# Kernel optimization log

Hardware: AMD Instinct MI355X
Metric: run time of the kernel (lower is better)

## Reference

```python
import jax, jax.numpy as jnp
import numpy as np

NEG_BIG = -1e9

def setup_inputs() -> dict:
    key = jax.random.key(0)
    kq, kk, kv, kwq, kwk, kwv, km = jax.random.split(key, 7)
    B, S, d = 16, 1024, 512
    Q = jax.random.normal(kq, (B, S, d), dtype=jnp.float32)
    K = jax.random.normal(kk, (B, S, d), dtype=jnp.float32)
    V = jax.random.normal(kv, (B, S, d), dtype=jnp.float32)
    # nn.Linear weights [d, d]; torch applies x @ W.T
    WQ = jax.random.normal(kwq, (d, d), dtype=jnp.float32) / np.sqrt(d)
    WK = jax.random.normal(kwk, (d, d), dtype=jnp.float32) / np.sqrt(d)
    WV = jax.random.normal(kwv, (d, d), dtype=jnp.float32) / np.sqrt(d)
    mask = jax.random.randint(km, (B, S), 0, 2, dtype=jnp.int32)
    return {"Q": Q, "K": K, "V": V, "WQ": WQ, "WK": WK, "WV": WV, "mask": mask}


def reference(Q, K, V, WQ, WK, WV, mask):
    d = Q.shape[-1]
    q = jnp.einsum('bsd,ed->bse', Q, WQ)
    k = jnp.einsum('bsd,ed->bse', K, WK)
    v = jnp.einsum('bsd,ed->bse', V, WV)
    scores = jnp.einsum('bqd,bkd->bqk', q, k) / jnp.sqrt(jnp.float32(d))
    attn = jax.nn.softmax(scores, axis=-1)
    # Faithful to original: mask applied AFTER softmax with -1e9 fill
    m = mask[:, None, :]  # [B,1,S] broadcast over query dim
    attn = jnp.where(m == 0, jnp.float32(NEG_BIG), attn)
    out = jnp.einsum('bqk,bkd->bqd', attn, v)
    return (out, attn)
```

## Files before the change

kernel.cpp:

```cpp
#include <hip/hip_runtime.h>
#include <hip/hip_bf16.h>

typedef float f32x4 __attribute__((ext_vector_type(4)));
typedef __bf16 bf16x8 __attribute__((ext_vector_type(8)));
typedef unsigned short u16x8 __attribute__((ext_vector_type(8)));
typedef unsigned short u16x4 __attribute__((ext_vector_type(4)));
typedef int i32x4 __attribute__((ext_vector_type(4)));

#define NEG_BIG_F (-1000000000.0f)
#define SCALE_F 0.044194173824159216f

__device__ __forceinline__ unsigned short f2bf(float f) {
  unsigned int u = __float_as_uint(f);
  u += 0x7FFFu + ((u >> 16) & 1u);
  return (unsigned short)(u >> 16);
}

__device__ __forceinline__ float bf2f(unsigned short h) {
  return __uint_as_float((unsigned int)h << 16);
}

__device__ __forceinline__ u16x8 cvt8(f32x4 a, f32x4 b) {
  u16x8 r;
  r[0] = f2bf(a[0]); r[1] = f2bf(a[1]); r[2] = f2bf(a[2]); r[3] = f2bf(a[3]);
  r[4] = f2bf(b[0]); r[5] = f2bf(b[1]); r[6] = f2bf(b[2]); r[7] = f2bf(b[3]);
  return r;
}

__device__ __forceinline__ void gload16(const void* g, char* l) {
  __builtin_amdgcn_global_load_lds(
      (const __attribute__((address_space(1))) unsigned int*)g,
      (__attribute__((address_space(3))) unsigned int*)l, 16, 0, 0);
}

__global__ __launch_bounds__(256) void cvtW(
    const float* __restrict__ w0, const float* __restrict__ w1,
    const float* __restrict__ w2, unsigned short* __restrict__ out)
{
  const float* src = blockIdx.z == 0 ? w0 : (blockIdx.z == 1 ? w1 : w2);
  unsigned short* dst = out + (size_t)blockIdx.z * 262144;
  const int i = (blockIdx.x * 256 + threadIdx.x) * 8;
  f32x4 a = *(const f32x4*)(src + i);
  f32x4 b = *(const f32x4*)(src + i + 4);
  *(u16x8*)&dst[i] = cvt8(a, b);
}

__global__ __launch_bounds__(512, 2) void proj_all(
    const float* __restrict__ Q, const float* __restrict__ Kx,
    const float* __restrict__ V, const unsigned short* __restrict__ wb,
    unsigned short* __restrict__ qb, unsigned short* __restrict__ kb,
    unsigned short* __restrict__ vt)
{
  __shared__ __align__(16) unsigned short lds[32768];

  const int bid = blockIdx.x;
  const int tid = threadIdx.x;
  const int lane = tid & 63, wave = tid >> 6;
  const int fr = lane & 15, fq = lane >> 4;

  if (bid < 256) {
    const int z = bid >> 7, rem = bid & 127;
    const float* X = z ? Kx : Q;
    const unsigned short* W = wb + (size_t)z * 262144;
    unsigned short* Y = z ? kb : qb;
    const int m0 = (rem & 63) * 256, n0 = (rem >> 6) * 256;
    const int wr = (wave >> 2) * 128, wc = (wave & 3) * 64;

    unsigned short (*As)[256][32] = (unsigned short (*)[256][32])lds;
    unsigned short (*Bs)[256][32] = (unsigned short (*)[256][32])(lds + 16384);

    f32x4 acc[8][4] = {};

    int arow_s[2], aswz_s[2];
    const float* gAs[2];
    #pragma unroll
    for (int i = 0; i < 2; i++) {
      const int c = tid + 512 * i;
      arow_s[i] = c >> 2;
      aswz_s[i] = ((c & 3) ^ ((arow_s[i] >> 1) & 3)) * 8;
      gAs[i] = X + (size_t)(m0 + arow_s[i]) * 512 + (c & 3) * 8;
    }
    const unsigned short* gB[2]; char* lB[2];
    #pragma unroll
    for (int i = 0; i < 2; i++) {
      const int c = tid + 512 * i, row = c >> 2, slot = c & 3;
      gB[i] = W + (size_t)(n0 + row) * 512 + (slot ^ ((row >> 1) & 3)) * 8;
      lB[i] = (char*)(lds + 16384) + c * 16;
    }

    f32x4 pa[2][2][2];
    #pragma unroll
    for (int i = 0; i < 2; i++) {
      pa[0][i][0] = *(const f32x4*)(gAs[i]);
      pa[0][i][1] = *(const f32x4*)(gAs[i] + 4);
      pa[1][i][0] = *(const f32x4*)(gAs[i] + 32);
      pa[1][i][1] = *(const f32x4*)(gAs[i] + 36);
    }
    #pragma unroll
    for (int i = 0; i < 2; i++) gload16(gB[i], lB[i]);
    #pragma unroll
    for (int i = 0; i < 2; i++)
      *(u16x8*)&As[0][arow_s[i]][aswz_s[i]] = cvt8(pa[0][i][0], pa[0][i][1]);

    #pragma unroll
    for (int t = 0; t < 16; t++) {
      const int cur = t & 1, nxt = cur ^ 1;
      const int kt = t * 32;
      if (t < 15) {
        #pragma unroll
        for (int i = 0; i < 2; i++) gload16(gB[i] + kt + 32, lB[i] + nxt * 16384);
      }
      if (t < 14) {
        #pragma unroll
        for (int i = 0; i < 2; i++) {
          pa[cur][i][0] = *(const f32x4*)(gAs[i] + kt + 64);
          pa[cur][i][1] = *(const f32x4*)(gAs[i] + kt + 68);
        }
      }
      if (t == 0 || t == 14)
        asm volatile("s_waitcnt vmcnt(6) lgkmcnt(0)" ::: "memory");
      else if (t == 15)
        asm volatile("s_waitcnt vmcnt(0) lgkmcnt(0)" ::: "memory");
      else
        asm volatile("s_waitcnt vmcnt(10) lgkmcnt(0)" ::: "memory");
      __builtin_amdgcn_sched_barrier(0);
      __builtin_amdgcn_s_barrier();

      bf16x8 bv[4];
      #pragma unroll
      for (int nf = 0; nf < 4; nf++) {
        const int br = wc + nf * 16 + fr;
        bv[nf] = *(const bf16x8*)&Bs[cur][br][(fq ^ ((br >> 1) & 3)) * 8];
      }
      #pragma unroll
      for (int mf = 0; mf < 8; mf++) {
        const int ar = wr + mf * 16 + fr;
        bf16x8 av = *(const bf16x8*)&As[cur][ar][(fq ^ ((ar >> 1) & 3)) * 8];
        #pragma unroll
        for (int nf = 0; nf < 4; nf++)
          acc[mf][nf] = __builtin_amdgcn_mfma_f32_16x16x32_bf16(av, bv[nf], acc[mf][nf], 0, 0, 0);
      }

      if (t < 15) {
        #pragma unroll
        for (int i = 0; i < 2; i++)
          *(u16x8*)&As[nxt][arow_s[i]][aswz_s[i]] = cvt8(pa[nxt][i][0], pa[nxt][i][1]);
      }
      __builtin_amdgcn_s_barrier();
    }

    #pragma unroll
    for (int mf = 0; mf < 8; mf++)
      #pragma unroll
      for (int nf = 0; nf < 4; nf++)
        #pragma unroll
        for (int rr = 0; rr < 4; rr++) {
          const int m = m0 + wr + mf * 16 + fq * 4 + rr;
          const int n = n0 + wc + nf * 16 + fr;
          Y[(size_t)m * 512 + n] = f2bf(acc[mf][nf][rr]);
        }
  } else {
    const int c0 = bid - 256;
    const int m0 = (c0 & 3) * 128, n0 = ((c0 >> 2) & 3) * 256, b = c0 >> 4;
    const int wr = (wave >> 2) * 64, wc = (wave & 3) * 64;
    const unsigned short* wv = wb + 524288;

    unsigned short (*As)[128][32] = (unsigned short (*)[128][32])lds;
    unsigned short (*Bs)[256][32] = (unsigned short (*)[256][32])(lds + 8192);

    f32x4 acc[4][4] = {};

    const int ar_s = tid >> 2, aslot = tid & 3;
    const unsigned short* gA = wv + (size_t)(m0 + ar_s) * 512 + (aslot ^ ((ar_s >> 1) & 3)) * 8;
    char* lA = (char*)lds + tid * 16;

    int brow_s[2], bswz_s[2];
    const float* gBs[2];
    #pragma unroll
    for (int i = 0; i < 2; i++) {
      const int c = tid + 512 * i;
      brow_s[i] = c >> 2;
      bswz_s[i] = ((c & 3) ^ ((brow_s[i] >> 1) & 3)) * 8;
      gBs[i] = V + ((size_t)b * 1024 + n0 + brow_s[i]) * 512 + (c & 3) * 8;
    }

    f32x4 pb[2][2][2];
    #pragma unroll
    for (int i = 0; i < 2; i++) {
      pb[0][i][0] = *(const f32x4*)(gBs[i]);
      pb[0][i][1] = *(const f32x4*)(gBs[i] + 4);
      pb[1][i][0] = *(const f32x4*)(gBs[i] + 32);
      pb[1][i][1] = *(const f32x4*)(gBs[i] + 36);
    }
    gload16(gA, lA);
    #pragma unroll
    for (int i = 0; i < 2; i++)
      *(u16x8*)&Bs[0][brow_s[i]][bswz_s[i]] = cvt8(pb[0][i][0], pb[0][i][1]);

    #pragma unroll
    for (int t = 0; t < 16; t++) {
      const int cur = t & 1, nxt = cur ^ 1;
      const int kt = t * 32;
      if (t < 15) gload16(gA + kt + 32, lA + nxt * 8192);
      if (t < 14) {
        #pragma unroll
        for (int i = 0; i < 2; i++) {
          pb[cur][i][0] = *(const f32x4*)(gBs[i] + kt + 64);
          pb[cur][i][1] = *(const f32x4*)(gBs[i] + kt + 68);
        }
      }
      if (t == 0 || t == 14)
        asm volatile("s_waitcnt vmcnt(5) lgkmcnt(0)" ::: "memory");
      else if (t == 15)
        asm volatile("s_waitcnt vmcnt(0) lgkmcnt(0)" ::: "memory");
      else
        asm volatile("s_waitcnt vmcnt(9) lgkmcnt(0)" ::: "memory");
      __builtin_amdgcn_sched_barrier(0);
      __builtin_amdgcn_s_barrier();

      bf16x8 av[4], bv[4];
      #pragma unroll
      for (int mf = 0; mf < 4; mf++) {
        const int ar = wr + mf * 16 + fr;
        av[mf] = *(const bf16x8*)&As[cur][ar][(fq ^ ((ar >> 1) & 3)) * 8];
      }
      #pragma unroll
      for (int nf = 0; nf < 4; nf++) {
        const int br = wc + nf * 16 + fr;
        bv[nf] = *(const bf16x8*)&Bs[cur][br][(fq ^ ((br >> 1) & 3)) * 8];
      }
      #pragma unroll
      for (int mf = 0; mf < 4; mf++)
        #pragma unroll
        for (int nf = 0; nf < 4; nf++)
          acc[mf][nf] = __builtin_amdgcn_mfma_f32_16x16x32_bf16(av[mf], bv[nf], acc[mf][nf], 0, 0, 0);

      if (t < 15) {
        #pragma unroll
        for (int i = 0; i < 2; i++)
          *(u16x8*)&Bs[nxt][brow_s[i]][bswz_s[i]] = cvt8(pb[nxt][i][0], pb[nxt][i][1]);
      }
      __builtin_amdgcn_s_barrier();
    }

    #pragma unroll
    for (int mf = 0; mf < 4; mf++)
      #pragma unroll
      for (int nf = 0; nf < 4; nf++)
        #pragma unroll
        for (int rr = 0; rr < 4; rr++) {
          const int e = m0 + wr + mf * 16 + fq * 4 + rr;
          const int s = n0 + wc + nf * 16 + fr;
          vt[((size_t)b * 512 + e) * 1024 + s] = f2bf(acc[mf][nf][rr]);
        }
  }
}

__global__ __launch_bounds__(512, 2) void score_mv(
    const unsigned short* __restrict__ qb, const unsigned short* __restrict__ kb,
    const unsigned short* __restrict__ vt, const int* __restrict__ mask,
    unsigned short* __restrict__ P, float* __restrict__ partial,
    float* __restrict__ mvsum)
{
  __shared__ __align__(16) unsigned short As[2][256][32];
  __shared__ __align__(16) unsigned short Bs[2][256][32];

  const int bid = blockIdx.x;
  const int tid = threadIdx.x;

  if (bid >= 256) {
    const int row = (bid - 256) * 8 + (tid >> 6);
    const int b = row >> 9;
    const int lane = tid & 63;
    const unsigned short* vr = vt + (size_t)row * 1024 + lane * 16;
    const int* mr = mask + b * 1024 + lane * 16;
    u16x8 v0 = *(const u16x8*)(vr);
    u16x8 v1 = *(const u16x8*)(vr + 8);
    float s = 0.f;
    #pragma unroll
    for (int j = 0; j < 8; j++) {
      if (!mr[j])     s += bf2f(v0[j]);
      if (!mr[8 + j]) s += bf2f(v1[j]);
    }
    #pragma unroll
    for (int o = 32; o > 0; o >>= 1) s += __shfl_xor(s, o);
    if (lane == 0) mvsum[row] = s;
    return;
  }

  const int bz = bid >> 4;
  const int m0 = (bid & 3) * 256, n0 = ((bid >> 2) & 3) * 256;
  const int lane = tid & 63, wave = tid >> 6;
  const int wr = (wave >> 2) * 128, wc = (wave & 3) * 64;
  const int fr = lane & 15, fq = lane >> 4;

  f32x4 acc[8][4] = {};

  const unsigned short* gA[2]; char* lA[2];
  const unsigned short* gB[2]; char* lB[2];
  #pragma unroll
  for (int i = 0; i < 2; i++) {
    const int c = tid + 512 * i, row = c >> 2, slot = c & 3;
    const int sw = (slot ^ ((row >> 1) & 3)) * 8;
    gA[i] = qb + ((size_t)bz * 1024 + m0 + row) * 512 + sw;
    gB[i] = kb + ((size_t)bz * 1024 + n0 + row) * 512 + sw;
    lA[i] = (char*)&As[0][0][0] + c * 16;
    lB[i] = (char*)&Bs[0][0][0] + c * 16;
  }

  #pragma unroll
  for (int i = 0; i < 2; i++) { gload16(gA[i], lA[i]); gload16(gB[i], lB[i]); }

  int cur = 0;
  for (int kt = 0; kt < 512; kt += 32) {
    const int nb = cur ^ 1;
    if (kt < 480) {
      #pragma unroll
      for (int i = 0; i < 2; i++) {
        gload16(gA[i] + kt + 32, lA[i] + nb * 16384);
        gload16(gB[i] + kt + 32, lB[i] + nb * 16384);
      }
      asm volatile("s_waitcnt vmcnt(4) lgkmcnt(0)" ::: "memory");
    } else {
      asm volatile("s_waitcnt vmcnt(0) lgkmcnt(0)" ::: "memory");
    }
    __builtin_amdgcn_sched_barrier(0);
    __builtin_amdgcn_s_barrier();

    bf16x8 bv[4];
    #pragma unroll
    for (int nf = 0; nf < 4; nf++) {
      const int br = wc + nf * 16 + fr;
      bv[nf] = *(const bf16x8*)&Bs[cur][br][(fq ^ ((br >> 1) & 3)) * 8];
    }
    #pragma unroll
    for (int mf = 0; mf < 8; mf++) {
      const int ar = wr + mf * 16 + fr;
      bf16x8 av = *(const bf16x8*)&As[cur][ar][(fq ^ ((ar >> 1) & 3)) * 8];
      #pragma unroll
      for (int nf = 0; nf < 4; nf++)
        acc[mf][nf] = __builtin_amdgcn_mfma_f32_16x16x32_bf16(av, bv[nf], acc[mf][nf], 0, 0, 0);
    }
    __builtin_amdgcn_s_barrier();
    cur = nb;
  }

  int mcol[4];
  #pragma unroll
  for (int nf = 0; nf < 4; nf++)
    mcol[nf] = mask[bz * 1024 + n0 + wc + nf * 16 + fr];

  unsigned short* Pb = P + ((size_t)bz << 20);
  const int slot = ((bid >> 2) & 3) * 4 + (wave & 3);
  #pragma unroll
  for (int mf = 0; mf < 8; mf++) {
    #pragma unroll
    for (int rr = 0; rr < 4; rr++) {
      const int m = m0 + wr + mf * 16 + fq * 4 + rr;
      float e = 0.f;
      #pragma unroll
      for (int nf = 0; nf < 4; nf++) {
        const float ev = __expf(acc[mf][nf][rr] * SCALE_F);
        e += ev;
        Pb[(size_t)m * 1024 + n0 + wc + nf * 16 + fr] =
            mcol[nf] ? f2bf(ev) : (unsigned short)0;
      }
      e += __shfl_xor(e, 1); e += __shfl_xor(e, 2);
      e += __shfl_xor(e, 4); e += __shfl_xor(e, 8);
      if (fr == 0)
        partial[(size_t)slot * 16384 + bz * 1024 + m] = e;
    }
  }
}

__global__ __launch_bounds__(512) void pv_attn(
    const unsigned short* __restrict__ P, const unsigned short* __restrict__ vt,
    const float* __restrict__ partial, const float* __restrict__ mvsum,
    const int* __restrict__ mask,
    float* __restrict__ out, float* __restrict__ attn)
{
  __shared__ __align__(16) unsigned short As[2][64][32];
  __shared__ __align__(16) unsigned short Bs[2][512][32];
  __shared__ float inv_l[64];

  const int tid = threadIdx.x;
  const int bz = blockIdx.z, m0 = blockIdx.x * 64;
  const int lane = tid & 63, wave = tid >> 6;
  const int n0 = wave * 64;
  const int fr = lane & 15, fq = lane >> 4;

  f32x4 acc[4][4] = {};

  if (tid < 64) {
    float s = 0.f;
    #pragma unroll
    for (int p = 0; p < 16; p++) s += partial[(size_t)p * 16384 + bz * 1024 + m0 + tid];
    inv_l[tid] = 1.0f / s;
  }

  const unsigned short* gA = nullptr; char* lA = nullptr;
  if (tid < 256) {
    const int row = tid >> 2, slot = tid & 3;
    gA = P + ((size_t)bz << 20) + (size_t)(m0 + row) * 1024 + (slot ^ ((row >> 1) & 3)) * 8;
    lA = (char*)&As[0][0][0] + tid * 16;
  }
  const unsigned short* gB[4]; char* lB[4];
  #pragma unroll
  for (int i = 0; i < 4; i++) {
    const int c = tid + 512 * i, row = c >> 2, slot = c & 3;
    gB[i] = vt + ((size_t)bz * 512 + row) * 1024 + (slot ^ ((row >> 1) & 3)) * 8;
    lB[i] = (char*)&Bs[0][0][0] + c * 16;
  }

  const int arow = tid >> 3, acol = (tid & 7) * 4;
  const int aslot8 = ((acol >> 3) ^ ((arow >> 1) & 3)) * 8 + (acol & 7);
  float* arp = attn + ((size_t)bz * 1024 + m0 + arow) * 1024 + acol;
  const int* mrp = mask + bz * 1024 + acol;

  if (tid < 256) gload16(gA, lA);
  #pragma unroll
  for (int i = 0; i < 4; i++) gload16(gB[i], lB[i]);
  __syncthreads();

  int cur = 0;
  for (int t = 0; t < 32; t++) {
    const int nb = cur ^ 1;
    const int kt = t * 32;
    if (t < 31) {
      if (tid < 256) gload16(gA + kt + 32, lA + nb * 4096);
      #pragma unroll
      for (int i = 0; i < 4; i++) gload16(gB[i] + kt + 32, lB[i] + nb * 32768);
      if (wave < 4) asm volatile("s_waitcnt vmcnt(5) lgkmcnt(0)" ::: "memory");
      else          asm volatile("s_waitcnt vmcnt(4) lgkmcnt(0)" ::: "memory");
    } else {
      asm volatile("s_waitcnt vmcnt(0) lgkmcnt(0)" ::: "memory");
    }
    __builtin_amdgcn_sched_barrier(0);
    __builtin_amdgcn_s_barrier();

    bf16x8 af[4], bv[4];
    #pragma unroll
    for (int mf = 0; mf < 4; mf++) {
      const int ar = mf * 16 + fr;
      af[mf] = *(const bf16x8*)&As[cur][ar][(fq ^ ((ar >> 1) & 3)) * 8];
    }
    #pragma unroll
    for (int nf = 0; nf < 4; nf++) {
      const int br = n0 + nf * 16 + fr;
      bv[nf] = *(const bf16x8*)&Bs[cur][br][(fq ^ ((br >> 1) & 3)) * 8];
    }
    #pragma unroll
    for (int mf = 0; mf < 4; mf++)
      #pragma unroll
      for (int nf = 0; nf < 4; nf++)
        acc[mf][nf] = __builtin_amdgcn_mfma_f32_16x16x32_bf16(af[mf], bv[nf], acc[mf][nf], 0, 0, 0);

    {
      const u16x4 pv4 = *(const u16x4*)&As[cur][arow][aslot8];
      const i32x4 mv = *(const i32x4*)(mrp + kt);
      const float iv = inv_l[arow];
      f32x4 o;
      o[0] = mv[0] ? bf2f(pv4[0]) * iv : NEG_BIG_F;
      o[1] = mv[1] ? bf2f(pv4[1]) * iv : NEG_BIG_F;
      o[2] = mv[2] ? bf2f(pv4[2]) * iv : NEG_BIG_F;
      o[3] = mv[3] ? bf2f(pv4[3]) * iv : NEG_BIG_F;
      *(f32x4*)(arp + kt) = o;
    }
    __builtin_amdgcn_s_barrier();
    cur = nb;
  }

  float mvv[4];
  #pragma unroll
  for (int nf = 0; nf < 4; nf++)
    mvv[nf] = mvsum[bz * 512 + n0 + nf * 16 + fr];
  #pragma unroll
  for (int mf = 0; mf < 4; mf++)
    #pragma unroll
    for (int rr = 0; rr < 4; rr++) {
      const int m = m0 + mf * 16 + fq * 4 + rr;
      const float iv = inv_l[mf * 16 + fq * 4 + rr];
      #pragma unroll
      for (int nf = 0; nf < 4; nf++)
        out[((size_t)bz * 1024 + m) * 512 + n0 + nf * 16 + fr] =
            iv * acc[mf][nf][rr] + NEG_BIG_F * mvv[nf];
    }
}

extern "C" void kernel_launch(void* const* d_in, const int* in_sizes, int n_in,
                              void* d_out, int out_size, void* d_ws, size_t ws_size,
                              hipStream_t stream)
{
  const float* Q  = (const float*)d_in[0];
  const float* Kx = (const float*)d_in[1];
  const float* V  = (const float*)d_in[2];
  const float* WQ = (const float*)d_in[3];
  const float* WK = (const float*)d_in[4];
  const float* WV = (const float*)d_in[5];
  const int* mask = (const int*)d_in[6];

  const int B = 16, S = 1024, D = 512;
  float* out_f  = (float*)d_out;
  float* attn_f = out_f + (size_t)B * S * D;
  unsigned short* Pbuf = (unsigned short*)d_out;

  unsigned short* qb = (unsigned short*)d_ws;
  unsigned short* kb = qb + (size_t)B * S * D;
  unsigned short* vt = kb + (size_t)B * S * D;
  unsigned short* wb = vt + (size_t)B * S * D;
  float* partial = (float*)(wb + 786432);
  float* mvsum = partial + 262144;

  cvtW<<<dim3(128, 1, 3), 256, 0, stream>>>(WQ, WK, WV, wb);
  proj_all<<<dim3(512), 512, 0, stream>>>(Q, Kx, V, wb, qb, kb, vt);
  score_mv<<<dim3(1280), 512, 0, stream>>>(qb, kb, vt, mask, Pbuf, partial, mvsum);
  pv_attn<<<dim3(16, 1, 16), 512, 0, stream>>>(Pbuf, vt, partial, mvsum, mask, out_f, attn_f);
}
```

Before: 143.3 us.

## Pre-convert Q/K/V inputs to bf16 and unify projection GEMM tiles

Adds a conversion pass that writes bf16 copies of Q, K and V into the attn output region used as scratch. The projection kernel then loads both operands asynchronously straight into LDS instead of doing register-staged fp32 loads with in-loop conversion. The V-projection path now uses the same 256x256 tile shape as Q/K, which reduces the grid from 512 to 384 blocks. In exchange the extra pass costs a full fp32 read plus bf16 write of all inputs, and there are fewer blocks to fill the device.

```diff
diff --git a/kernel.cpp b/kernel.cpp
--- a/kernel.cpp
+++ b/kernel.cpp
@@ -33,122 +33,115 @@
       (__attribute__((address_space(3))) unsigned int*)l, 16, 0, 0);
 }
 
-__global__ __launch_bounds__(256) void cvtW(
+__global__ __launch_bounds__(256) void cvtWX(
     const float* __restrict__ w0, const float* __restrict__ w1,
-    const float* __restrict__ w2, unsigned short* __restrict__ out)
+    const float* __restrict__ w2, const float* __restrict__ Q,
+    const float* __restrict__ Kx, const float* __restrict__ V,
+    unsigned short* __restrict__ wb, unsigned short* __restrict__ xb)
 {
-  const float* src = blockIdx.z == 0 ? w0 : (blockIdx.z == 1 ? w1 : w2);
-  unsigned short* dst = out + (size_t)blockIdx.z * 262144;
-  const int i = (blockIdx.x * 256 + threadIdx.x) * 8;
-  f32x4 a = *(const f32x4*)(src + i);
-  f32x4 b = *(const f32x4*)(src + i + 4);
-  *(u16x8*)&dst[i] = cvt8(a, b);
+  const int z = blockIdx.z;
+  if (z == 0) {
+    if (blockIdx.x >= 384) return;
+    const int i = (blockIdx.x * 256 + threadIdx.x) * 8;
+    const float* src = i < 262144 ? w0 : (i < 524288 ? w1 : w2);
+    const int j = i & 262143;
+    f32x4 a = *(const f32x4*)(src + j);
+    f32x4 b = *(const f32x4*)(src + j + 4);
+    *(u16x8*)&wb[i] = cvt8(a, b);
+  } else {
+    const float* src = z == 1 ? Q : (z == 2 ? Kx : V);
+    unsigned short* dst = xb + (size_t)(z - 1) * 8388608;
+    const int i = (blockIdx.x * 256 + threadIdx.x) * 8;
+    f32x4 a = *(const f32x4*)(src + i);
+    f32x4 b = *(const f32x4*)(src + i + 4);
+    *(u16x8*)&dst[i] = cvt8(a, b);
+  }
 }
 
 __global__ __launch_bounds__(512, 2) void proj_all(
-    const float* __restrict__ Q, const float* __restrict__ Kx,
-    const float* __restrict__ V, const unsigned short* __restrict__ wb,
+    const unsigned short* __restrict__ xb, const unsigned short* __restrict__ wb,
     unsigned short* __restrict__ qb, unsigned short* __restrict__ kb,
     unsigned short* __restrict__ vt)
 {
-  __shared__ __align__(16) unsigned short lds[32768];
+  __shared__ __align__(16) unsigned short As[2][256][32];
+  __shared__ __align__(16) unsigned short Bs[2][256][32];
 
   const int bid = blockIdx.x;
   const int tid = threadIdx.x;
   const int lane = tid & 63, wave = tid >> 6;
+  const int wr = (wave >> 2) * 128, wc = (wave & 3) * 64;
   const int fr = lane & 15, fq = lane >> 4;
 
+  const unsigned short* Abase;
+  const unsigned short* Bbase;
+  int m0, n0;
   if (bid < 256) {
     const int z = bid >> 7, rem = bid & 127;
-    const float* X = z ? Kx : Q;
-    const unsigned short* W = wb + (size_t)z * 262144;
-    unsigned short* Y = z ? kb : qb;
-    const int m0 = (rem & 63) * 256, n0 = (rem >> 6) * 256;
-    const int wr = (wave >> 2) * 128, wc = (wave & 3) * 64;
-
-    unsigned short (*As)[256][32] = (unsigned short (*)[256][32])lds;
-    unsigned short (*Bs)[256][32] = (unsigned short (*)[256][32])(lds + 16384);
-
-    f32x4 acc[8][4] = {};
-
-    int arow_s[2], aswz_s[2];
-    const float* gAs[2];
-    #pragma unroll
-    for (int i = 0; i < 2; i++) {
-      const int c = tid + 512 * i;
-      arow_s[i] = c >> 2;
-      aswz_s[i] = ((c & 3) ^ ((arow_s[i] >> 1) & 3)) * 8;
-      gAs[i] = X + (size_t)(m0 + arow_s[i]) * 512 + (c & 3) * 8;
-    }
-    const unsigned short* gB[2]; char* lB[2];
-    #pragma unroll
-    for (int i = 0; i < 2; i++) {
-      const int c = tid + 512 * i, row = c >> 2, slot = c & 3;
-      gB[i] = W + (size_t)(n0 + row) * 512 + (slot ^ ((row >> 1) & 3)) * 8;
-      lB[i] = (char*)(lds + 16384) + c * 16;
-    }
-
-    f32x4 pa[2][2][2];
-    #pragma unroll
-    for (int i = 0; i < 2; i++) {
-      pa[0][i][0] = *(const f32x4*)(gAs[i]);
-      pa[0][i][1] = *(const f32x4*)(gAs[i] + 4);
-      pa[1][i][0] = *(const f32x4*)(gAs[i] + 32);
-      pa[1][i][1] = *(const f32x4*)(gAs[i] + 36);
-    }
-    #pragma unroll
-    for (int i = 0; i < 2; i++) gload16(gB[i], lB[i]);
-    #pragma unroll
-    for (int i = 0; i < 2; i++)
-      *(u16x8*)&As[0][arow_s[i]][aswz_s[i]] = cvt8(pa[0][i][0], pa[0][i][1]);
-
-    #pragma unroll
-    for (int t = 0; t < 16; t++) {
-      const int cur = t & 1, nxt = cur ^ 1;
-      const int kt = t * 32;
-      if (t < 15) {
-        #pragma unroll
-        for (int i = 0; i < 2; i++) gload16(gB[i] + kt + 32, lB[i] + nxt * 16384);
+    m0 = (rem & 63) * 256; n0 = (rem >> 6) * 256;
+    Abase = xb + (size_t)z * 8388608 + (size_t)m0 * 512;
+    Bbase = wb + (size_t)z * 262144 + (size_t)n0 * 512;
+  } else {
+    const int c0 = bid - 256;
+    const int b = c0 >> 3;
+    m0 = ((c0 >> 2) & 1) * 256;
+    n0 = (c0 & 3) * 256;
+    Abase = wb + 524288 + (size_t)m0 * 512;
+    Bbase = xb + 16777216 + ((size_t)b * 1024 + n0) * 512;
+  }
+
+  f32x4 acc[8][4] = {};
+
+  const unsigned short* gA[2]; char* lA[2];
+  const unsigned short* gB[2]; char* lB[2];
+  #pragma unroll
+  for (int i = 0; i < 2; i++) {
+    const int c = tid + 512 * i, row = c >> 2, slot = c & 3;
+    const int sw = (slot ^ ((row >> 1) & 3)) * 8;
+    gA[i] = Abase + (size_t)row * 512 + sw;
+    gB[i] = Bbase + (size_t)row * 512 + sw;
+    lA[i] = (char*)&As[0][0][0] + c * 16;
+    lB[i] = (char*)&Bs[0][0][0] + c * 16;
+  }
+
+  #pragma unroll
+  for (int i = 0; i < 2; i++) { gload16(gA[i], lA[i]); gload16(gB[i], lB[i]); }
+
+  int cur = 0;
+  for (int kt = 0; kt < 512; kt += 32) {
+    const int nb = cur ^ 1;
+    if (kt < 480) {
+      #pragma unroll
+      for (int i = 0; i < 2; i++) {
+        gload16(gA[i] + kt + 32, lA[i] + nb * 16384);
+        gload16(gB[i] + kt + 32, lB[i] + nb * 16384);
       }
-      if (t < 14) {
-        #pragma unroll
-        for (int i = 0; i < 2; i++) {
-          pa[cur][i][0] = *(const f32x4*)(gAs[i] + kt + 64);
-          pa[cur][i][1] = *(const f32x4*)(gAs[i] + kt + 68);
-        }
-      }
-      if (t == 0 || t == 14)
-        asm volatile("s_waitcnt vmcnt(6) lgkmcnt(0)" ::: "memory");
-      else if (t == 15)
-        asm volatile("s_waitcnt vmcnt(0) lgkmcnt(0)" ::: "memory");
-      else
-        asm volatile("s_waitcnt vmcnt(10) lgkmcnt(0)" ::: "memory");
-      __builtin_amdgcn_sched_barrier(0);
-      __builtin_amdgcn_s_barrier();
-
-      bf16x8 bv[4];
-      #pragma unroll
-      for (int nf = 0; nf < 4; nf++) {
-        const int br = wc + nf * 16 + fr;
-        bv[nf] = *(const bf16x8*)&Bs[cur][br][(fq ^ ((br >> 1) & 3)) * 8];
-      }
-      #pragma unroll
-      for (int mf = 0; mf < 8; mf++) {
-        const int ar = wr + mf * 16 + fr;
-        bf16x8 av = *(const bf16x8*)&As[cur][ar][(fq ^ ((ar >> 1) & 3)) * 8];
-        #pragma unroll
-        for (int nf = 0; nf < 4; nf++)
-          acc[mf][nf] = __builtin_amdgcn_mfma_f32_16x16x32_bf16(av, bv[nf], acc[mf][nf], 0, 0, 0);
-      }
-
-      if (t < 15) {
-        #pragma unroll
-        for (int i = 0; i < 2; i++)
-          *(u16x8*)&As[nxt][arow_s[i]][aswz_s[i]] = cvt8(pa[nxt][i][0], pa[nxt][i][1]);
-      }
-      __builtin_amdgcn_s_barrier();
-    }
-
+      asm volatile("s_waitcnt vmcnt(4) lgkmcnt(0)" ::: "memory");
+    } else {
+      asm volatile("s_waitcnt vmcnt(0) lgkmcnt(0)" ::: "memory");
+    }
+    __builtin_amdgcn_sched_barrier(0);
+    __builtin_amdgcn_s_barrier();
+
+    bf16x8 bv[4];
+    #pragma unroll
+    for (int nf = 0; nf < 4; nf++) {
+      const int br = wc + nf * 16 + fr;
+      bv[nf] = *(const bf16x8*)&Bs[cur][br][(fq ^ ((br >> 1) & 3)) * 8];
+    }
+    #pragma unroll
+    for (int mf = 0; mf < 8; mf++) {
+      const int ar = wr + mf * 16 + fr;
+      bf16x8 av = *(const bf16x8*)&As[cur][ar][(fq ^ ((ar >> 1) & 3)) * 8];
+      #pragma unroll
+      for (int nf = 0; nf < 4; nf++)
+        acc[mf][nf] = __builtin_amdgcn_mfma_f32_16x16x32_bf16(av, bv[nf], acc[mf][nf], 0, 0, 0);
+    }
+    __builtin_amdgcn_s_barrier();
+    cur = nb;
+  }
+
+  if (bid < 256) {
+    unsigned short* Y = (bid >> 7) ? kb : qb;
     #pragma unroll
     for (int mf = 0; mf < 8; mf++)
       #pragma unroll
@@ -160,91 +153,9 @@
           Y[(size_t)m * 512 + n] = f2bf(acc[mf][nf][rr]);
         }
   } else {
-    const int c0 = bid - 256;
-    const int m0 = (c0 & 3) * 128, n0 = ((c0 >> 2) & 3) * 256, b = c0 >> 4;
-    const int wr = (wave >> 2) * 64, wc = (wave & 3) * 64;
-    const unsigned short* wv = wb + 524288;
-
-    unsigned short (*As)[128][32] = (unsigned short (*)[128][32])lds;
-    unsigned short (*Bs)[256][32] = (unsigned short (*)[256][32])(lds + 8192);
-
-    f32x4 acc[4][4] = {};
-
-    const int ar_s = tid >> 2, aslot = tid & 3;
-    const unsigned short* gA = wv + (size_t)(m0 + ar_s) * 512 + (aslot ^ ((ar_s >> 1) & 3)) * 8;
-    char* lA = (char*)lds + tid * 16;
-
-    int brow_s[2], bswz_s[2];
-    const float* gBs[2];
-    #pragma unroll
-    for (int i = 0; i < 2; i++) {
-      const int c = tid + 512 * i;
-      brow_s[i] = c >> 2;
-      bswz_s[i] = ((c & 3) ^ ((brow_s[i] >> 1) & 3)) * 8;
-      gBs[i] = V + ((size_t)b * 1024 + n0 + brow_s[i]) * 512 + (c & 3) * 8;
-    }
-
-    f32x4 pb[2][2][2];
-    #pragma unroll
-    for (int i = 0; i < 2; i++) {
-      pb[0][i][0] = *(const f32x4*)(gBs[i]);
-      pb[0][i][1] = *(const f32x4*)(gBs[i] + 4);
-      pb[1][i][0] = *(const f32x4*)(gBs[i] + 32);
-      pb[1][i][1] = *(const f32x4*)(gBs[i] + 36);
-    }
-    gload16(gA, lA);
-    #pragma unroll
-    for (int i = 0; i < 2; i++)
-      *(u16x8*)&Bs[0][brow_s[i]][bswz_s[i]] = cvt8(pb[0][i][0], pb[0][i][1]);
-
-    #pragma unroll
-    for (int t = 0; t < 16; t++) {
-      const int cur = t & 1, nxt = cur ^ 1;
-      const int kt = t * 32;
-      if (t < 15) gload16(gA + kt + 32, lA + nxt * 8192);
-      if (t < 14) {
-        #pragma unroll
-        for (int i = 0; i < 2; i++) {
-          pb[cur][i][0] = *(const f32x4*)(gBs[i] + kt + 64);
-          pb[cur][i][1] = *(const f32x4*)(gBs[i] + kt + 68);
-        }
-      }
-      if (t == 0 || t == 14)
-        asm volatile("s_waitcnt vmcnt(5) lgkmcnt(0)" ::: "memory");
-      else if (t == 15)
-        asm volatile("s_waitcnt vmcnt(0) lgkmcnt(0)" ::: "memory");
-      else
-        asm volatile("s_waitcnt vmcnt(9) lgkmcnt(0)" ::: "memory");
-      __builtin_amdgcn_sched_barrier(0);
-      __builtin_amdgcn_s_barrier();
-
-      bf16x8 av[4], bv[4];
-      #pragma unroll
-      for (int mf = 0; mf < 4; mf++) {
-        const int ar = wr + mf * 16 + fr;
-        av[mf] = *(const bf16x8*)&As[cur][ar][(fq ^ ((ar >> 1) & 3)) * 8];
-      }
-      #pragma unroll
-      for (int nf = 0; nf < 4; nf++) {
-        const int br = wc + nf * 16 + fr;
-        bv[nf] = *(const bf16x8*)&Bs[cur][br][(fq ^ ((br >> 1) & 3)) * 8];
-      }
-      #pragma unroll
-      for (int mf = 0; mf < 4; mf++)
-        #pragma unroll
-        for (int nf = 0; nf < 4; nf++)
-          acc[mf][nf] = __builtin_amdgcn_mfma_f32_16x16x32_bf16(av[mf], bv[nf], acc[mf][nf], 0, 0, 0);
-
-      if (t < 15) {
-        #pragma unroll
-        for (int i = 0; i < 2; i++)
-          *(u16x8*)&Bs[nxt][brow_s[i]][bswz_s[i]] = cvt8(pb[nxt][i][0], pb[nxt][i][1]);
-      }
-      __builtin_amdgcn_s_barrier();
-    }
-
-    #pragma unroll
-    for (int mf = 0; mf < 4; mf++)
+    const int b = (bid - 256) >> 3;
+    #pragma unroll
+    for (int mf = 0; mf < 8; mf++)
       #pragma unroll
       for (int nf = 0; nf < 4; nf++)
         #pragma unroll
@@ -503,6 +414,7 @@
   float* out_f  = (float*)d_out;
   float* attn_f = out_f + (size_t)B * S * D;
   unsigned short* Pbuf = (unsigned short*)d_out;
+  unsigned short* xb = (unsigned short*)attn_f;
 
   unsigned short* qb = (unsigned short*)d_ws;
   unsigned short* kb = qb + (size_t)B * S * D;
@@ -511,8 +423,8 @@
   float* partial = (float*)(wb + 786432);
   float* mvsum = partial + 262144;
 
-  cvtW<<<dim3(128, 1, 3), 256, 0, stream>>>(WQ, WK, WV, wb);
-  proj_all<<<dim3(512), 512, 0, stream>>>(Q, Kx, V, wb, qb, kb, vt);
+  cvtWX<<<dim3(4096, 1, 4), 256, 0, stream>>>(WQ, WK, WV, Q, Kx, V, wb, xb);
+  proj_all<<<dim3(384), 512, 0, stream>>>(xb, wb, qb, kb, vt);
   score_mv<<<dim3(1280), 512, 0, stream>>>(qb, kb, vt, mask, Pbuf, partial, mvsum);
   pv_attn<<<dim3(16, 1, 16), 512, 0, stream>>>(Pbuf, vt, partial, mvsum, mask, out_f, attn_f);
 }
```

Result: no change. 144.5 us (+0.8%).
